# Kernel optimization log

Hardware: AMD Instinct MI355X
Metric: run time of the kernel (lower is better)

## Reference

```python
import jax, jax.numpy as jnp
from jax import lax
import numpy as np

B, T, C = 4, 1024, 1024
NH, HS = 16, 64
K, STRIDE = 32, 16
EPS = 1e-5


def _ln(x, w, b):
    m = jnp.mean(x, axis=-1, keepdims=True)
    v = jnp.mean((x - m) ** 2, axis=-1, keepdims=True)
    return (x - m) * lax.rsqrt(v + EPS) * w + b


def setup_inputs() -> dict:
    key = jax.random.key(0)
    ks = jax.random.split(key, 12)
    s = 0.02
    return {
        'x': jax.random.normal(ks[0], (B, T, C), jnp.float32),
        'c_attn_w': jax.random.normal(ks[1], (C, 3 * C), jnp.float32) * s,
        'c_attn_b': jnp.zeros((3 * C,), jnp.float32),
        'c_proj_w': jax.random.normal(ks[2], (C, C), jnp.float32) * s,
        'c_proj_b': jnp.zeros((C,), jnp.float32),
        'conv_w': jax.random.normal(ks[3], (HS, HS, K), jnp.float32) * s,  # OIH
        'conv_b': jnp.zeros((HS,), jnp.float32),
        'comp_ln_w': jnp.ones((HS,), jnp.float32),
        'comp_ln_b': jnp.zeros((HS,), jnp.float32),
        'ln_local_w': jnp.ones((C,), jnp.float32),
        'ln_local_b': jnp.zeros((C,), jnp.float32),
        'gate_w1': jax.random.normal(ks[4], (2 * C, C), jnp.float32) * s,
        'gate_b1': jnp.zeros((C,), jnp.float32),
        'gate_ln_w': jnp.ones((C,), jnp.float32),
        'gate_ln_b': jnp.zeros((C,), jnp.float32),
        'gate_w2': jax.random.normal(ks[5], (C, 2), jnp.float32) * s,
        'gate_b2': jnp.zeros((2,), jnp.float32),
    }


def _compress(h, conv_w, conv_b, comp_ln_w, comp_ln_b):
    # h: [B, nh, T, hs] -> [B, nh, num_blocks, hs]
    b, nh, t, hs = h.shape
    xr = h.transpose(0, 1, 3, 2).reshape(b * nh, hs, t)  # NCH
    co = lax.conv_general_dilated(xr, conv_w, (STRIDE,), 'VALID',
                                  dimension_numbers=('NCH', 'OIH', 'NCH'))
    co = co + conv_b[None, :, None]
    y = co.transpose(0, 2, 1)  # [B*nh, nb, hs]
    y = _ln(y, comp_ln_w, comp_ln_b)
    y = jax.nn.gelu(y, approximate=False)
    return y.reshape(b, nh, -1, hs)


def _attn(q, k, v, mask):
    # q:[B,nh,T,hs] k,v:[B,nh,Tk,hs], mask:[T,Tk] bool (True=keep)
    scale = 1.0 / jnp.sqrt(jnp.asarray(q.shape[-1], q.dtype))
    att = jnp.einsum('bhqd,bhkd->bhqk', q, k) * scale
    att = jnp.where(mask[None, None], att, jnp.finfo(att.dtype).min)
    att = jax.nn.softmax(att, axis=-1)
    return jnp.einsum('bhqk,bhkd->bhqd', att, v)


def reference(x, c_attn_w, c_attn_b, c_proj_w, c_proj_b, conv_w, conv_b,
              comp_ln_w, comp_ln_b, ln_local_w, ln_local_b,
              gate_w1, gate_b1, gate_ln_w, gate_ln_b, gate_w2, gate_b2):
    b, t, c = x.shape
    qkv = x @ c_attn_w + c_attn_b
    q, k, v = jnp.split(qkv, 3, axis=-1)
    q = q.reshape(b, t, NH, HS).transpose(0, 2, 1, 3)
    k = k.reshape(b, t, NH, HS).transpose(0, 2, 1, 3)
    v = v.reshape(b, t, NH, HS).transpose(0, 2, 1, 3)

    k_comp = _compress(k, conv_w, conv_b, comp_ln_w, comp_ln_b)
    v_comp = _compress(v, conv_w, conv_b, comp_ln_w, comp_ln_b)
    nb = k_comp.shape[2]

    # local branch: flash path with is_causal=True skips the window mask -> plain causal
    causal = jnp.tril(jnp.ones((t, t), bool))
    local = _attn(q, k, v, causal)
    local = local.transpose(0, 2, 1, 3).reshape(b, t, c)
    local_norm = _ln(local, ln_local_w, ln_local_b)

    # compressed branch: causal mask of shape [T, num_blocks], diagonal 0
    comp_mask = jnp.tril(jnp.ones((t, nb), bool), k=0)
    comp = _attn(q, k_comp, v_comp, comp_mask)
    comp = comp.transpose(0, 2, 1, 3).reshape(b, t, c)

    # gating from last-token features
    feats = jnp.concatenate([local_norm[:, -1, :], comp[:, -1, :]], axis=-1)  # [B, 2C]
    h = jax.nn.relu(_ln(feats @ gate_w1 + gate_b1, gate_ln_w, gate_ln_b))
    gates = jax.nn.softmax(h @ gate_w2 + gate_b2, axis=-1)  # [B, 2]
    g = gates[:, None, :]  # [B, 1, 2]
    combined = g[..., 0:1] * local_norm + g[..., 1:2] * comp

    return combined @ c_proj_w + c_proj_b
```

## Files before the change

### kernel.cpp

```cpp
#include <hip/hip_runtime.h>

using u16 = unsigned short;
using f32x4 = __attribute__((ext_vector_type(4))) float;
using s16x8 = __attribute__((ext_vector_type(8))) short;
using u16x4 = __attribute__((ext_vector_type(4))) unsigned short;

__device__ __forceinline__ u16 f2bf(float f) {
  unsigned u = __float_as_uint(f);
  return (u16)((u + 0x7FFFu + ((u >> 16) & 1u)) >> 16);
}

__device__ __forceinline__ f32x4 mfma16(s16x8 a, s16x8 b, f32x4 c) {
  return __builtin_amdgcn_mfma_f32_16x16x32_bf16(a, b, c, 0, 0, 0);
}

__device__ __forceinline__ void gld16(const void* g, void* l) {
  __builtin_amdgcn_global_load_lds(
      (const __attribute__((address_space(1))) unsigned int*)g,
      (__attribute__((address_space(3))) unsigned int*)l, 16, 0, 0);
}

__global__ __launch_bounds__(256) void cast_bf16(const float* __restrict__ in,
                                                 u16* __restrict__ out, int n4) {
  int i = blockIdx.x * 256 + threadIdx.x;
  if (i >= n4) return;
  f32x4 v = *(const f32x4*)(in + (size_t)i * 4);
  u16x4 o = {f2bf(v[0]), f2bf(v[1]), f2bf(v[2]), f2bf(v[3])};
  *(u16x4*)(out + (size_t)i * 4) = o;
}

__global__ __launch_bounds__(256) void transpose_cast(const float* __restrict__ in,
                                                      u16* __restrict__ out,
                                                      int R, int C) {
  __shared__ float t[32][33];
  int bx = blockIdx.x, by = blockIdx.y;
  int tx = threadIdx.x & 31, ty = threadIdx.x >> 5;
#pragma unroll
  for (int r = 0; r < 4; r++) {
    int row = by * 32 + ty + r * 8;
    t[ty + r * 8][tx] = in[(size_t)row * C + bx * 32 + tx];
  }
  __syncthreads();
#pragma unroll
  for (int r = 0; r < 4; r++) {
    int orow = bx * 32 + ty + r * 8;
    out[(size_t)orow * R + by * 32 + tx] = f2bf(t[tx][ty + r * 8]);
  }
}

__device__ __forceinline__ void gemm_mainloop(const u16* A, const u16* Bt, int K,
                                              u16* As, u16* Bs, f32x4 acc[4][4]) {
  const int tid = threadIdx.x;
  const int row = tid >> 2, c16 = tid & 3;
  const int lane = tid & 63, wid = tid >> 6;
  const int wm = wid >> 1, wn = wid & 1, lg = lane >> 4, lr = lane & 15;
  const u16* ga = A + (size_t)row * K + c16 * 8;
  const u16* gb = Bt + (size_t)row * K + c16 * 8;
  const size_t rowskip = (size_t)64 * K;
  for (int k0 = 0; k0 < K; k0 += 32) {
    gld16(ga + k0, As + tid * 8);
    gld16(ga + rowskip + k0, As + 2048 + tid * 8);
    gld16(gb + k0, Bs + tid * 8);
    gld16(gb + rowskip + k0, Bs + 2048 + tid * 8);
    __syncthreads();
    s16x8 af[4], bfr[4];
#pragma unroll
    for (int i = 0; i < 4; i++)
      af[i] = *(const s16x8*)(As + (wm * 64 + i * 16 + lr) * 32 + lg * 8);
#pragma unroll
    for (int j = 0; j < 4; j++)
      bfr[j] = *(const s16x8*)(Bs + (wn * 64 + j * 16 + lr) * 32 + lg * 8);
#pragma unroll
    for (int i = 0; i < 4; i++)
#pragma unroll
      for (int j = 0; j < 4; j++) acc[i][j] = mfma16(af[i], bfr[j], acc[i][j]);
    __syncthreads();
  }
}

__global__ __launch_bounds__(256) void gemm_qkv(const u16* __restrict__ A,
                                                const u16* __restrict__ Bt,
                                                const float* __restrict__ bias,
                                                u16* __restrict__ qo, u16* __restrict__ ko,
                                                u16* __restrict__ kTo, u16* __restrict__ vTo) {
  __shared__ u16 As[4096];
  __shared__ u16 Bs[4096];
  int m0 = blockIdx.x * 128, n0 = blockIdx.y * 128;
  f32x4 acc[4][4] = {};
  gemm_mainloop(A + (size_t)m0 * 1024, Bt + (size_t)n0 * 1024, 1024, As, Bs, acc);
  int lane = threadIdx.x & 63, wid = threadIdx.x >> 6;
  int wm = wid >> 1, wn = wid & 1, lg = lane >> 4, lr = lane & 15;
#pragma unroll
  for (int i = 0; i < 4; i++) {
    int mb = m0 + wm * 64 + i * 16 + lg * 4;
    int b = mb >> 10, tb = mb & 1023;
#pragma unroll
    for (int j = 0; j < 4; j++) {
      int n = n0 + wn * 64 + j * 16 + lr;
      float bs = bias[n];
      int sel = n >> 10, hd = n & 1023, h = hd >> 6, d = hd & 63;
      int bh = b * 16 + h;
      u16 u0 = f2bf(acc[i][j][0] + bs), u1 = f2bf(acc[i][j][1] + bs);
      u16 u2 = f2bf(acc[i][j][2] + bs), u3 = f2bf(acc[i][j][3] + bs);
      if (sel == 0) {
        u16* qp = qo + ((size_t)bh << 16) + ((size_t)tb << 6) + d;
        qp[0] = u0; qp[64] = u1; qp[128] = u2; qp[192] = u3;
      } else if (sel == 1) {
        u16* kp = ko + ((size_t)bh << 16) + ((size_t)tb << 6) + d;
        kp[0] = u0; kp[64] = u1; kp[128] = u2; kp[192] = u3;
        u16x4 pk = {u0, u1, u2, u3};
        *(u16x4*)(kTo + ((size_t)(bh * 64 + d) << 10) + tb) = pk;
      } else {
        u16x4 pk = {u0, u1, u2, u3};
        *(u16x4*)(vTo + ((size_t)(bh * 64 + d) << 10) + tb) = pk;
      }
    }
  }
}

__global__ __launch_bounds__(256) void gemm_proj(const u16* __restrict__ A,
                                                 const u16* __restrict__ Bt,
                                                 const float* __restrict__ bias,
                                                 float* __restrict__ out) {
  __shared__ u16 As[4096];
  __shared__ u16 Bs[4096];
  int m0 = blockIdx.x * 128, n0 = blockIdx.y * 128;
  f32x4 acc[4][4] = {};
  gemm_mainloop(A + (size_t)m0 * 1024, Bt + (size_t)n0 * 1024, 1024, As, Bs, acc);
  int lane = threadIdx.x & 63, wid = threadIdx.x >> 6;
  int wm = wid >> 1, wn = wid & 1, lg = lane >> 4, lr = lane & 15;
#pragma unroll
  for (int i = 0; i < 4; i++) {
    int mb = m0 + wm * 64 + i * 16 + lg * 4;
#pragma unroll
    for (int j = 0; j < 4; j++) {
      int n = n0 + wn * 64 + j * 16 + lr;
      float bs = bias[n];
#pragma unroll
      for (int r = 0; r < 4; r++)
        out[(size_t)(mb + r) * 1024 + n] = acc[i][j][r] + bs;
    }
  }
}

__global__ __launch_bounds__(256) void conv_comp(const u16* __restrict__ kT,
                                                 const u16* __restrict__ vT,
                                                 const u16* __restrict__ cw,
                                                 const float* __restrict__ cb,
                                                 const float* __restrict__ lnw,
                                                 const float* __restrict__ lnb,
                                                 u16* __restrict__ kcomp,
                                                 u16* __restrict__ vcompT) {
  int bh = blockIdx.x, sel = blockIdx.y;
  const u16* src = (sel ? vT : kT) + ((size_t)bh << 16);
  int tid = threadIdx.x, wid = tid >> 6, lane = tid & 63, lg = lane >> 4, lr = lane & 15;
  f32x4 acc[4] = {};
  int arow = wid * 16 + lr;
  if (arow > 62) arow = 62;
  const u16* abase = src + (size_t)arow * 16 + lg * 8;
#pragma unroll 4
  for (int ic = 0; ic < 64; ic++) {
    s16x8 a = *(const s16x8*)(abase + ic * 1024);
#pragma unroll
    for (int j = 0; j < 4; j++) {
      s16x8 bfr = *(const s16x8*)(cw + (size_t)(j * 16 + lr) * 2048 + ic * 32 + lg * 8);
      acc[j] = mfma16(a, bfr, acc[j]);
    }
  }
  float lwv[4], lbv[4];
#pragma unroll
  for (int j = 0; j < 4; j++) {
    int oc = j * 16 + lr;
    float cbv = cb[oc];
    acc[j][0] += cbv; acc[j][1] += cbv; acc[j][2] += cbv; acc[j][3] += cbv;
    lwv[j] = lnw[oc]; lbv[j] = lnb[oc];
  }
#pragma unroll
  for (int r = 0; r < 4; r++) {
    float s = acc[0][r] + acc[1][r] + acc[2][r] + acc[3][r];
    float q = acc[0][r] * acc[0][r] + acc[1][r] * acc[1][r] +
              acc[2][r] * acc[2][r] + acc[3][r] * acc[3][r];
#pragma unroll
    for (int off = 1; off < 16; off <<= 1) {
      s += __shfl_xor(s, off);
      q += __shfl_xor(q, off);
    }
    float mean = s * (1.f / 64.f);
    float var = q * (1.f / 64.f) - mean * mean;
    float rstd = rsqrtf(fmaxf(var, 0.f) + 1e-5f);
    int op = wid * 16 + lg * 4 + r;
#pragma unroll
    for (int j = 0; j < 4; j++) {
      float y = (acc[j][r] - mean) * rstd * lwv[j] + lbv[j];
      y = 0.5f * y * (1.0f + erff(y * 0.70710678118f));
      if (op > 62) y = 0.f;
      int oc = j * 16 + lr;
      if (sel == 0) kcomp[((size_t)bh << 12) + (op << 6) + oc] = f2bf(y);
      else          vcompT[((size_t)bh << 12) + (oc << 6) + op] = f2bf(y);
    }
  }
}

__global__ __launch_bounds__(256) void flash64(const u16* __restrict__ qg,
                                               const u16* __restrict__ kg,
                                               const u16* __restrict__ vg,
                                               float* __restrict__ outg,
                                               int k_bh, int v_bh, int vrow, int kvmax) {
  __shared__ u16 Ks[2][4096];
  __shared__ u16 Vs[2][4096];
  __shared__ u16 Pl[4][1152];
  const int tid = threadIdx.x;
  const int w = tid >> 6, lane = tid & 63, lg = lane >> 4, lr = lane & 15;
  const int qt0 = gridDim.x - 1 - blockIdx.x;
  const int bh = blockIdx.y;
  const int q0 = qt0 * 64;
  const int qrow = q0 + w * 16 + lr;
  const u16* qb = qg + ((size_t)bh << 16) + (size_t)qrow * 64 + lg * 8;
  s16x8 qf0 = *(const s16x8*)(qb);
  s16x8 qf1 = *(const s16x8*)(qb + 32);
  const u16* kb = kg + (size_t)bh * k_bh;
  const u16* vb = vg + (size_t)bh * v_bh;
  int nt = qt0 + 1;
  int ntk = (kvmax + 63) >> 6;
  if (nt > ntk) nt = ntk;
  u16* Pw = Pl[w];
  f32x4 ot[4] = {};
  float m = -INFINITY, l = 0.f;

  auto stage = [&](int bufi, int kv0) {
#pragma unroll
    for (int rnd = 0; rnd < 2; rnd++) {
      int o = tid * 16 + rnd * 4096;
      int row = o >> 7;
      int sb = (o & 127) ^ ((row & 7) << 4);
      gld16(kb + (size_t)(kv0 + row) * 64 + (sb >> 1), &Ks[bufi][o >> 1]);
      gld16(vb + (size_t)row * vrow + kv0 + (sb >> 1), &Vs[bufi][o >> 1]);
    }
  };

  stage(0, 0);
  int cur = 0;
  for (int t = 0; t < nt; t++) {
    __syncthreads();
    if (t + 1 < nt) stage(cur ^ 1, (t + 1) * 64);
    const int kv0 = t * 64;
    const u16* Kb = Ks[cur];
    const u16* Vb = Vs[cur];
    f32x4 st[4];
    __builtin_amdgcn_s_setprio(1);
#pragma unroll
    for (int kvt = 0; kvt < 4; kvt++) {
      int rr = kvt * 16 + lr;
      int sw = (rr & 7) << 4;
      s16x8 k0 = *(const s16x8*)(Kb + (((rr << 7) + ((lg * 16) ^ sw)) >> 1));
      s16x8 k1 = *(const s16x8*)(Kb + (((rr << 7) + ((64 + lg * 16) ^ sw)) >> 1));
      f32x4 z = {};
      z = mfma16(k0, qf0, z);
      z = mfma16(k1, qf1, z);
      st[kvt] = z;
    }
    __builtin_amdgcn_s_setprio(0);
    float p[16];
    float tm = -INFINITY;
#pragma unroll
    for (int kvt = 0; kvt < 4; kvt++)
#pragma unroll
      for (int r = 0; r < 4; r++) {
        int kvi = kv0 + kvt * 16 + lg * 4 + r;
        float v = st[kvt][r] * 0.125f;
        v = (kvi <= qrow && kvi < kvmax) ? v : -INFINITY;
        p[kvt * 4 + r] = v;
        tm = fmaxf(tm, v);
      }
    tm = fmaxf(tm, __shfl_xor(tm, 16));
    tm = fmaxf(tm, __shfl_xor(tm, 32));
    float mnew = fmaxf(m, tm);
    float fac = __expf(m - mnew);
    float ls = 0.f;
#pragma unroll
    for (int i = 0; i < 16; i++) {
      float e = __expf(p[i] - mnew);
      p[i] = e;
      ls += e;
    }
    ls += __shfl_xor(ls, 16);
    ls += __shfl_xor(ls, 32);
    l = l * fac + ls;
    m = mnew;
#pragma unroll
    for (int d4 = 0; d4 < 4; d4++) {
      ot[d4][0] *= fac; ot[d4][1] *= fac; ot[d4][2] *= fac; ot[d4][3] *= fac;
    }
#pragma unroll
    for (int kvt = 0; kvt < 4; kvt++) {
      unsigned w0 = (unsigned)f2bf(p[kvt * 4 + 0]) | ((unsigned)f2bf(p[kvt * 4 + 1]) << 16);
      unsigned w1 = (unsigned)f2bf(p[kvt * 4 + 2]) | ((unsigned)f2bf(p[kvt * 4 + 3]) << 16);
      uint2 pk = {w0, w1};
      *(uint2*)(Pw + lr * 72 + kvt * 16 + lg * 4) = pk;
    }
    s16x8 bp0 = *(const s16x8*)(Pw + lr * 72 + lg * 8);
    s16x8 bp1 = *(const s16x8*)(Pw + lr * 72 + 32 + lg * 8);
    __builtin_amdgcn_s_setprio(1);
#pragma unroll
    for (int d4 = 0; d4 < 4; d4++) {
      int dr = d4 * 16 + lr;
      int sw = (dr & 7) << 4;
      s16x8 v0 = *(const s16x8*)(Vb + (((dr << 7) + ((lg * 16) ^ sw)) >> 1));
      s16x8 v1 = *(const s16x8*)(Vb + (((dr << 7) + ((64 + lg * 16) ^ sw)) >> 1));
      ot[d4] = mfma16(v0, bp0, ot[d4]);
      ot[d4] = mfma16(v1, bp1, ot[d4]);
    }
    __builtin_amdgcn_s_setprio(0);
    cur ^= 1;
  }
  float inv = 1.f / l;
  int b = bh >> 4, h = bh & 15;
  float* op = outg + ((size_t)((b << 10) + qrow) << 10) + h * 64;
#pragma unroll
  for (int d4 = 0; d4 < 4; d4++) {
    f32x4 v;
#pragma unroll
    for (int c = 0; c < 4; c++) v[c] = ot[d4][c] * inv;
    *(f32x4*)(op + d4 * 16 + lg * 4) = v;
  }
}

__global__ __launch_bounds__(256) void ln_rows(float* __restrict__ x,
                                               const float* __restrict__ w,
                                               const float* __restrict__ b) {
  __shared__ float red[8];
  size_t row = blockIdx.x;
  float* xr = x + (row << 10);
  int tid = threadIdx.x;
  f32x4 v = *(const f32x4*)(xr + tid * 4);
  float s = v[0] + v[1] + v[2] + v[3];
  float q = v[0] * v[0] + v[1] * v[1] + v[2] * v[2] + v[3] * v[3];
#pragma unroll
  for (int off = 32; off >= 1; off >>= 1) {
    s += __shfl_xor(s, off);
    q += __shfl_xor(q, off);
  }
  int wid = tid >> 6;
  if ((tid & 63) == 0) { red[wid * 2] = s; red[wid * 2 + 1] = q; }
  __syncthreads();
  s = red[0] + red[2] + red[4] + red[6];
  q = red[1] + red[3] + red[5] + red[7];
  float mean = s * (1.0f / 1024.0f);
  float var = q * (1.0f / 1024.0f) - mean * mean;
  float rstd = rsqrtf(fmaxf(var, 0.f) + 1e-5f);
  f32x4 wv = *(const f32x4*)(w + tid * 4);
  f32x4 bv = *(const f32x4*)(b + tid * 4);
  f32x4 o;
#pragma unroll
  for (int c = 0; c < 4; c++) o[c] = (v[c] - mean) * rstd * wv[c] + bv[c];
  *(f32x4*)(xr + tid * 4) = o;
}

__global__ __launch_bounds__(256) void gate_partial(const float* __restrict__ ln,
                                                    const float* __restrict__ comp,
                                                    const float* __restrict__ w1,
                                                    float* __restrict__ partial) {
  __shared__ float f[4][32];
  int ib = blockIdx.x, i0 = ib * 32, tid = threadIdx.x;
  if (tid < 128) {
    int bb = tid >> 5, ii = tid & 31;
    int i = i0 + ii;
    const float* src = (i < 1024) ? ln : comp;
    int ic = i & 1023;
    f[bb][ii] = src[((size_t)(bb * 1024 + 1023) << 10) + ic];
  }
  __syncthreads();
  float acc[4][4] = {};
  for (int ii = 0; ii < 32; ii++) {
    float f0 = f[0][ii], f1 = f[1][ii], f2 = f[2][ii], f3 = f[3][ii];
#pragma unroll
    for (int jj = 0; jj < 4; jj++) {
      float w = w1[(size_t)(i0 + ii) * 1024 + jj * 256 + tid];
      acc[jj][0] += f0 * w; acc[jj][1] += f1 * w;
      acc[jj][2] += f2 * w; acc[jj][3] += f3 * w;
    }
  }
#pragma unroll
  for (int jj = 0; jj < 4; jj++)
#pragma unroll
    for (int bb = 0; bb < 4; bb++)
      partial[(size_t)((ib << 2) + bb) * 1024 + jj * 256 + tid] = acc[jj][bb];
}

__global__ __launch_bounds__(1024) void gate_finish(const float* __restrict__ partial,
                                                    const float* __restrict__ b1,
                                                    const float* __restrict__ lnw,
                                                    const float* __restrict__ lnb,
                                                    const float* __restrict__ w2,
                                                    const float* __restrict__ b2,
                                                    float* __restrict__ g) {
  __shared__ float redA[16], redB[16];
  int b = blockIdx.x, j = threadIdx.x;
  float s = b1[j];
#pragma unroll 4
  for (int ib = 0; ib < 64; ib++) s += partial[(size_t)((ib << 2) + b) * 1024 + j];
  float sa = s, sb = s * s;
#pragma unroll
  for (int off = 32; off >= 1; off >>= 1) {
    sa += __shfl_xor(sa, off);
    sb += __shfl_xor(sb, off);
  }
  int wid = j >> 6;
  if ((j & 63) == 0) { redA[wid] = sa; redB[wid] = sb; }
  __syncthreads();
  if (j == 0) {
    float A = 0, Bv = 0;
    for (int k2 = 0; k2 < 16; k2++) { A += redA[k2]; Bv += redB[k2]; }
    redA[0] = A; redB[0] = Bv;
  }
  __syncthreads();
  float S = redA[0], Q = redB[0];
  float mean = S * (1.f / 1024.f), var = Q * (1.f / 1024.f) - mean * mean;
  float rstd = rsqrtf(fmaxf(var, 0.f) + 1e-5f);
  float hn = (s - mean) * rstd * lnw[j] + lnb[j];
  hn = fmaxf(hn, 0.f);
  float c0 = hn * w2[j * 2], c1 = hn * w2[j * 2 + 1];
  __syncthreads();
  float ra = c0, rb = c1;
#pragma unroll
  for (int off = 32; off >= 1; off >>= 1) {
    ra += __shfl_xor(ra, off);
    rb += __shfl_xor(rb, off);
  }
  if ((j & 63) == 0) { redA[wid] = ra; redB[wid] = rb; }
  __syncthreads();
  if (j == 0) {
    float A = 0, Bv = 0;
    for (int k2 = 0; k2 < 16; k2++) { A += redA[k2]; Bv += redB[k2]; }
    A += b2[0]; Bv += b2[1];
    float mx = fmaxf(A, Bv);
    float e0 = __expf(A - mx), e1 = __expf(Bv - mx);
    float inv = 1.f / (e0 + e1);
    g[b * 2] = e0 * inv;
    g[b * 2 + 1] = e1 * inv;
  }
}

__global__ __launch_bounds__(256) void combine_k(const float* __restrict__ ln,
                                                 const float* __restrict__ comp,
                                                 const float* __restrict__ g,
                                                 u16* __restrict__ out) {
  size_t i = (size_t)blockIdx.x * 256 + threadIdx.x;
  size_t off = i << 2;
  int b = (int)(off >> 20);
  float g0 = g[b * 2], g1 = g[b * 2 + 1];
  f32x4 a = *(const f32x4*)(ln + off);
  f32x4 c = *(const f32x4*)(comp + off);
  u16x4 o = {f2bf(g0 * a[0] + g1 * c[0]), f2bf(g0 * a[1] + g1 * c[1]),
             f2bf(g0 * a[2] + g1 * c[2]), f2bf(g0 * a[3] + g1 * c[3])};
  *(u16x4*)(out + off) = o;
}

extern "C" void kernel_launch(void* const* d_in, const int* in_sizes, int n_in,
                              void* d_out, int out_size, void* d_ws, size_t ws_size,
                              hipStream_t stream) {
  const float* x        = (const float*)d_in[0];
  const float* c_attn_w = (const float*)d_in[1];
  const float* c_attn_b = (const float*)d_in[2];
  const float* c_proj_w = (const float*)d_in[3];
  const float* c_proj_b = (const float*)d_in[4];
  const float* conv_w   = (const float*)d_in[5];
  const float* conv_b   = (const float*)d_in[6];
  const float* comp_ln_w= (const float*)d_in[7];
  const float* comp_ln_b= (const float*)d_in[8];
  const float* ln_loc_w = (const float*)d_in[9];
  const float* ln_loc_b = (const float*)d_in[10];
  const float* gate_w1  = (const float*)d_in[11];
  const float* gate_b1  = (const float*)d_in[12];
  const float* gate_ln_w= (const float*)d_in[13];
  const float* gate_ln_b= (const float*)d_in[14];
  const float* gate_w2  = (const float*)d_in[15];
  const float* gate_b2  = (const float*)d_in[16];
  float* out = (float*)d_out;

  char* ws = (char*)d_ws;
  size_t off = 0;
  auto alloc = [&](size_t bytes) -> char* {
    char* p = ws + off;
    off += (bytes + 255) & ~(size_t)255;
    return p;
  };
  u16* x_bf     = (u16*)alloc(8388608);
  u16* attn_wT  = (u16*)alloc(6291456);
  u16* proj_wT  = (u16*)alloc(2097152);
  u16* conv_wbf = (u16*)alloc(262144);
  u16* q_bf     = (u16*)alloc(8388608);
  u16* k_bf     = (u16*)alloc(8388608);
  u16* kT_bf    = (u16*)alloc(8388608);
  u16* vT_bf    = (u16*)alloc(8388608);
  u16* k_comp   = (u16*)alloc(524288);
  u16* v_compT  = (u16*)alloc(524288);
  float* local  = (float*)alloc(16777216);
  float* comp   = (float*)alloc(16777216);
  float* partial= (float*)alloc(1048576);
  float* gbuf   = (float*)alloc(256);
  u16* combined = x_bf;
  if (off > ws_size) return;

  cast_bf16<<<dim3(4096), dim3(256), 0, stream>>>(x, x_bf, 1048576);
  transpose_cast<<<dim3(96, 32), dim3(256), 0, stream>>>(c_attn_w, attn_wT, 1024, 3072);
  transpose_cast<<<dim3(32, 32), dim3(256), 0, stream>>>(c_proj_w, proj_wT, 1024, 1024);
  cast_bf16<<<dim3(128), dim3(256), 0, stream>>>(conv_w, conv_wbf, 32768);

  gemm_qkv<<<dim3(32, 24), dim3(256), 0, stream>>>(x_bf, attn_wT, c_attn_b,
                                                   q_bf, k_bf, kT_bf, vT_bf);

  conv_comp<<<dim3(64, 2), dim3(256), 0, stream>>>(kT_bf, vT_bf, conv_wbf, conv_b,
                                                   comp_ln_w, comp_ln_b, k_comp, v_compT);

  flash64<<<dim3(16, 64), dim3(256), 0, stream>>>(q_bf, k_bf, vT_bf, local,
                                                  65536, 65536, 1024, 1024);
  flash64<<<dim3(16, 64), dim3(256), 0, stream>>>(q_bf, k_comp, v_compT, comp,
                                                  4096, 4096, 64, 63);

  ln_rows<<<dim3(4096), dim3(256), 0, stream>>>(local, ln_loc_w, ln_loc_b);

  gate_partial<<<dim3(64), dim3(256), 0, stream>>>(local, comp, gate_w1, partial);
  gate_finish<<<dim3(4), dim3(1024), 0, stream>>>(partial, gate_b1, gate_ln_w,
                                                  gate_ln_b, gate_w2, gate_b2, gbuf);

  combine_k<<<dim3(4096), dim3(256), 0, stream>>>(local, comp, gbuf, combined);
  gemm_proj<<<dim3(32, 8), dim3(256), 0, stream>>>(combined, proj_wT, c_proj_b, out);
}
```

Measured before the change: 310.4 us.

## Drop LDS staging in flash attention, remap blocks per XCD, skip rescale

The flash kernel no longer stages K and V tiles into shared memory with async global-to-LDS loads and barriers. Each wave now reads its MFMA operands straight from global memory and relies on L2/cache locality, helped by a 1D grid remapped so that blocks for the same head group land on the same XCD. It also adds a fast path with no causal masking for tiles that are fully visible, switches to exp2 with the log2e factor folded into the scale, and skips the running-max rescale when the max does not change. The trade is that each wave fetches K and V from global memory on its own, with no sharing through LDS and no double buffering, which costs extra memory traffic and latency.

```diff
diff --git a/kernel.cpp b/kernel.cpp
--- a/kernel.cpp
+++ b/kernel.cpp
@@ -206,13 +206,14 @@
                                                const u16* __restrict__ vg,
                                                float* __restrict__ outg,
                                                int k_bh, int v_bh, int vrow, int kvmax) {
-  __shared__ u16 Ks[2][4096];
-  __shared__ u16 Vs[2][4096];
   __shared__ u16 Pl[4][1152];
   const int tid = threadIdx.x;
   const int w = tid >> 6, lane = tid & 63, lg = lane >> 4, lr = lane & 15;
-  const int qt0 = gridDim.x - 1 - blockIdx.x;
-  const int bh = blockIdx.y;
+  const int idx = blockIdx.x;
+  const int nqt = gridDim.x >> 6;
+  const int xcd = idx & 7, j = idx >> 3;
+  const int bh = xcd * 8 + (j & 7);
+  const int qt0 = nqt - 1 - (j >> 3);
   const int q0 = qt0 * 64;
   const int qrow = q0 + w * 16 + lr;
   const u16* qb = qg + ((size_t)bh << 16) + (size_t)qrow * 64 + lg * 8;
@@ -226,71 +227,66 @@
   u16* Pw = Pl[w];
   f32x4 ot[4] = {};
   float m = -INFINITY, l = 0.f;
-
-  auto stage = [&](int bufi, int kv0) {
-#pragma unroll
-    for (int rnd = 0; rnd < 2; rnd++) {
-      int o = tid * 16 + rnd * 4096;
-      int row = o >> 7;
-      int sb = (o & 127) ^ ((row & 7) << 4);
-      gld16(kb + (size_t)(kv0 + row) * 64 + (sb >> 1), &Ks[bufi][o >> 1]);
-      gld16(vb + (size_t)row * vrow + kv0 + (sb >> 1), &Vs[bufi][o >> 1]);
-    }
-  };
-
-  stage(0, 0);
-  int cur = 0;
+  const float SCL = 0.125f * 1.44269504089f;
   for (int t = 0; t < nt; t++) {
-    __syncthreads();
-    if (t + 1 < nt) stage(cur ^ 1, (t + 1) * 64);
     const int kv0 = t * 64;
-    const u16* Kb = Ks[cur];
-    const u16* Vb = Vs[cur];
+    const bool full = (kv0 + 63 <= q0 + w * 16) && (kv0 + 64 <= kvmax);
     f32x4 st[4];
     __builtin_amdgcn_s_setprio(1);
 #pragma unroll
     for (int kvt = 0; kvt < 4; kvt++) {
-      int rr = kvt * 16 + lr;
-      int sw = (rr & 7) << 4;
-      s16x8 k0 = *(const s16x8*)(Kb + (((rr << 7) + ((lg * 16) ^ sw)) >> 1));
-      s16x8 k1 = *(const s16x8*)(Kb + (((rr << 7) + ((64 + lg * 16) ^ sw)) >> 1));
+      const u16* ka = kb + (size_t)(kv0 + kvt * 16 + lr) * 64 + lg * 8;
       f32x4 z = {};
-      z = mfma16(k0, qf0, z);
-      z = mfma16(k1, qf1, z);
+      z = mfma16(*(const s16x8*)(ka), qf0, z);
+      z = mfma16(*(const s16x8*)(ka + 32), qf1, z);
       st[kvt] = z;
     }
     __builtin_amdgcn_s_setprio(0);
     float p[16];
     float tm = -INFINITY;
-#pragma unroll
-    for (int kvt = 0; kvt < 4; kvt++)
-#pragma unroll
-      for (int r = 0; r < 4; r++) {
-        int kvi = kv0 + kvt * 16 + lg * 4 + r;
-        float v = st[kvt][r] * 0.125f;
-        v = (kvi <= qrow && kvi < kvmax) ? v : -INFINITY;
-        p[kvt * 4 + r] = v;
-        tm = fmaxf(tm, v);
-      }
+    if (full) {
+#pragma unroll
+      for (int kvt = 0; kvt < 4; kvt++)
+#pragma unroll
+        for (int r = 0; r < 4; r++) {
+          float v = st[kvt][r] * SCL;
+          p[kvt * 4 + r] = v;
+          tm = fmaxf(tm, v);
+        }
+    } else {
+#pragma unroll
+      for (int kvt = 0; kvt < 4; kvt++)
+#pragma unroll
+        for (int r = 0; r < 4; r++) {
+          int kvi = kv0 + kvt * 16 + lg * 4 + r;
+          float v = st[kvt][r] * SCL;
+          v = (kvi <= qrow && kvi < kvmax) ? v : -INFINITY;
+          p[kvt * 4 + r] = v;
+          tm = fmaxf(tm, v);
+        }
+    }
     tm = fmaxf(tm, __shfl_xor(tm, 16));
     tm = fmaxf(tm, __shfl_xor(tm, 32));
-    float mnew = fmaxf(m, tm);
-    float fac = __expf(m - mnew);
+    if (!__all(tm <= m)) {
+      float mnew = fmaxf(m, tm);
+      float fac = exp2f(m - mnew);
+      l *= fac;
+#pragma unroll
+      for (int d4 = 0; d4 < 4; d4++) {
+        ot[d4][0] *= fac; ot[d4][1] *= fac; ot[d4][2] *= fac; ot[d4][3] *= fac;
+      }
+      m = mnew;
+    }
     float ls = 0.f;
 #pragma unroll
     for (int i = 0; i < 16; i++) {
-      float e = __expf(p[i] - mnew);
+      float e = exp2f(p[i] - m);
       p[i] = e;
       ls += e;
     }
     ls += __shfl_xor(ls, 16);
     ls += __shfl_xor(ls, 32);
-    l = l * fac + ls;
-    m = mnew;
-#pragma unroll
-    for (int d4 = 0; d4 < 4; d4++) {
-      ot[d4][0] *= fac; ot[d4][1] *= fac; ot[d4][2] *= fac; ot[d4][3] *= fac;
-    }
+    l += ls;
 #pragma unroll
     for (int kvt = 0; kvt < 4; kvt++) {
       unsigned w0 = (unsigned)f2bf(p[kvt * 4 + 0]) | ((unsigned)f2bf(p[kvt * 4 + 1]) << 16);
@@ -303,15 +299,11 @@
     __builtin_amdgcn_s_setprio(1);
 #pragma unroll
     for (int d4 = 0; d4 < 4; d4++) {
-      int dr = d4 * 16 + lr;
-      int sw = (dr & 7) << 4;
-      s16x8 v0 = *(const s16x8*)(Vb + (((dr << 7) + ((lg * 16) ^ sw)) >> 1));
-      s16x8 v1 = *(const s16x8*)(Vb + (((dr << 7) + ((64 + lg * 16) ^ sw)) >> 1));
-      ot[d4] = mfma16(v0, bp0, ot[d4]);
-      ot[d4] = mfma16(v1, bp1, ot[d4]);
+      const u16* va = vb + (size_t)(d4 * 16 + lr) * vrow + kv0 + lg * 8;
+      ot[d4] = mfma16(*(const s16x8*)(va), bp0, ot[d4]);
+      ot[d4] = mfma16(*(const s16x8*)(va + 32), bp1, ot[d4]);
     }
     __builtin_amdgcn_s_setprio(0);
-    cur ^= 1;
   }
   float inv = 1.f / l;
   int b = bh >> 4, h = bh & 15;
@@ -513,10 +505,10 @@
   conv_comp<<<dim3(64, 2), dim3(256), 0, stream>>>(kT_bf, vT_bf, conv_wbf, conv_b,
                                                    comp_ln_w, comp_ln_b, k_comp, v_compT);
 
-  flash64<<<dim3(16, 64), dim3(256), 0, stream>>>(q_bf, k_bf, vT_bf, local,
-                                                  65536, 65536, 1024, 1024);
-  flash64<<<dim3(16, 64), dim3(256), 0, stream>>>(q_bf, k_comp, v_compT, comp,
-                                                  4096, 4096, 64, 63);
+  flash64<<<dim3(1024), dim3(256), 0, stream>>>(q_bf, k_bf, vT_bf, local,
+                                                65536, 65536, 1024, 1024);
+  flash64<<<dim3(1024), dim3(256), 0, stream>>>(q_bf, k_comp, v_compT, comp,
+                                                4096, 4096, 64, 63);
 
   ln_rows<<<dim3(4096), dim3(256), 0, stream>>>(local, ln_loc_w, ln_loc_b);
 
```

Result: slower. 334.1 us (+7.6%).
